# Kernel optimization log

Hardware: AMD Instinct MI355X
Metric: run time of the kernel (lower is better)

## Reference

```python
import jax, jax.numpy as jnp
import numpy as np

NUM_HEADS = 16
HEAD_DIM = 64  # hidden_size 1024 / 16 heads


def setup_inputs() -> dict:
    key = jax.random.key(0)
    ks = jax.random.split(key, 7)
    B, S, D = 32, 577, 1024
    s = 0.02
    return {
        "hidden_states": jax.random.normal(ks[0], (B, S, D), dtype=jnp.float32),
        "Wq": jax.random.normal(ks[1], (D, D), dtype=jnp.float32) * s,
        "bq": jax.random.normal(ks[2], (D,), dtype=jnp.float32) * s,
        "Wk": jax.random.normal(ks[3], (D, D), dtype=jnp.float32) * s,
        "bk": jax.random.normal(ks[4], (D,), dtype=jnp.float32) * s,
        "Wv": jax.random.normal(ks[5], (D, D), dtype=jnp.float32) * s,
        "bv": jax.random.normal(ks[6], (D,), dtype=jnp.float32) * s,
    }


def _split_heads(x):
    # [B, S, D] -> [B, H, S, d]
    B, S, D = x.shape
    return x.reshape(B, S, NUM_HEADS, HEAD_DIM).transpose(0, 2, 1, 3)


def reference(hidden_states, Wq, bq, Wk, bk, Wv, bv):
    # torch Linear: y = x @ W^T + b
    q = _split_heads(hidden_states @ Wq.T + bq)  # [B,H,S,d]
    k = _split_heads(hidden_states @ Wk.T + bk)
    v = _split_heads(hidden_states @ Wv.T + bv)

    scale = 1.0 / np.sqrt(HEAD_DIM).astype(np.float32)
    scores = jnp.einsum("bhqd,bhkd->bhqk", q, k) * scale  # [B,H,S,S]
    probs = jax.nn.softmax(scores, axis=-1)
    ctx = jnp.einsum("bhqk,bhkd->bhqd", probs, v)  # [B,H,S,d]
    B, H, S, d = ctx.shape
    ctx = ctx.transpose(0, 2, 1, 3).reshape(B, S, H * d)  # [B,S,D]
    return ctx
```

## Files before the change

kernel.cpp:

```cpp
#include <hip/hip_runtime.h>
#include <stdint.h>

#define NB 32
#define SEQ 577
#define SPAD 640
#define NH 16
#define HD 64
#define DM 1024
#define MTOT (NB * SEQ)
#define KT_N 16

typedef __bf16 bf16x8 __attribute__((ext_vector_type(8)));
typedef float f32x4 __attribute__((ext_vector_type(4)));
typedef unsigned short u16x8 __attribute__((ext_vector_type(8)));
typedef unsigned short u16x4 __attribute__((ext_vector_type(4)));

__device__ __forceinline__ unsigned short f2bf(float f) {
  unsigned int u = __builtin_bit_cast(unsigned int, f);
  return (unsigned short)((u + 0x7FFFu + ((u >> 16) & 1u)) >> 16);
}

__device__ __forceinline__ f32x4 mfma16(bf16x8 a, bf16x8 b, f32x4 c) {
  return __builtin_amdgcn_mfma_f32_16x16x32_bf16(a, b, c, 0, 0, 0);
}

__device__ __forceinline__ void gload16(const unsigned short* g, unsigned short* l) {
  __builtin_amdgcn_global_load_lds(
      (const __attribute__((address_space(1))) unsigned int*)g,
      (__attribute__((address_space(3))) unsigned int*)l, 16, 0, 0);
}

#define BC8(p) __builtin_bit_cast(bf16x8, *(const u16x8*)(p))

#if __has_builtin(__builtin_amdgcn_exp2f)
#define EXP2(x) __builtin_amdgcn_exp2f(x)
#else
#define EXP2(x) exp2f(x)
#endif

#define QSCALE 0.18033688f

__global__ void cvt_kernel(const float* __restrict__ x,
                           const float* __restrict__ wq,
                           const float* __restrict__ wk,
                           const float* __restrict__ wv,
                           unsigned short* __restrict__ xb,
                           unsigned short* __restrict__ wb) {
  const long long NX = (long long)MTOT * DM;
  long long i = ((long long)blockIdx.x * blockDim.x + threadIdx.x) * 4;
  const float* src;
  unsigned short* dst;
  if (i < NX) {
    src = x + i;
    dst = xb + i;
  } else {
    long long j = i - NX;
    int wsel = (int)(j >> 20);
    long long off = j & 0xFFFFF;
    src = (wsel == 0 ? wq : wsel == 1 ? wk : wv) + off;
    dst = wb + j;
  }
  f32x4 v = *(const f32x4*)src;
  u16x4 o;
  o.x = f2bf(v.x); o.y = f2bf(v.y); o.z = f2bf(v.z); o.w = f2bf(v.w);
  *(u16x4*)dst = o;
}

template <int MODE>
__device__ __forceinline__ void kloop256(
    unsigned short* LDS, const unsigned short* const* gA,
    const unsigned short* const* gB, f32x4 (&acc)[8][4],
    int rA0, int rB0, int ch0, int ch1) {
#define MM(ACC, AF, BF)                                   \
  do {                                                    \
    if constexpr (MODE == 0)                              \
      ACC = mfma16(AF, BF, ACC);                          \
    else                                                  \
      ACC = mfma16(BF, AF, ACC);                          \
  } while (0)
  const int t = threadIdx.x;
  for (int kt = 0; kt < KT_N; ++kt) {
    unsigned short* ab = LDS + (kt & 1) * 32768;
    unsigned short* bb = ab + 16384;
    const bool st = (kt + 2) < KT_N;
    const int ko2 = (kt + 2) * 64;
    bf16x8 af[4][2], bf0[2][2], bf1[2][2];

#pragma unroll
    for (int mi = 0; mi < 4; mi++) {
      const unsigned short* rp = ab + (rA0 + mi * 16) * 64;
      af[mi][0] = BC8(rp + ch0);
      af[mi][1] = BC8(rp + ch1);
    }
#pragma unroll
    for (int ni = 0; ni < 2; ni++) {
      const unsigned short* rp = bb + (rB0 + ni * 16) * 64;
      bf0[ni][0] = BC8(rp + ch0);
      bf0[ni][1] = BC8(rp + ch1);
    }
    __builtin_amdgcn_s_setprio(1);
#pragma unroll
    for (int mi = 0; mi < 4; mi++)
#pragma unroll
      for (int ni = 0; ni < 2; ni++) {
        MM(acc[mi][ni], af[mi][0], bf0[ni][0]);
        MM(acc[mi][ni], af[mi][1], bf0[ni][1]);
      }
    __builtin_amdgcn_s_setprio(0);
    asm volatile("s_waitcnt lgkmcnt(0)" ::: "memory");
    __builtin_amdgcn_s_barrier();
    __builtin_amdgcn_sched_barrier(0);

    if (st) {
      gload16(gA[0] + ko2, ab + 0 * 4096 + t * 8);
      gload16(gA[2] + ko2, ab + 2 * 4096 + t * 8);
    }
#pragma unroll
    for (int ni = 0; ni < 2; ni++) {
      const unsigned short* rp = bb + (rB0 + (2 + ni) * 16) * 64;
      bf1[ni][0] = BC8(rp + ch0);
      bf1[ni][1] = BC8(rp + ch1);
    }
    __builtin_amdgcn_s_setprio(1);
#pragma unroll
    for (int mi = 0; mi < 4; mi++)
#pragma unroll
      for (int ni = 0; ni < 2; ni++) {
        MM(acc[mi][2 + ni], af[mi][0], bf1[ni][0]);
        MM(acc[mi][2 + ni], af[mi][1], bf1[ni][1]);
      }
    __builtin_amdgcn_s_setprio(0);
    asm volatile("s_waitcnt lgkmcnt(0)" ::: "memory");
    __builtin_amdgcn_s_barrier();
    __builtin_amdgcn_sched_barrier(0);

    if (st) {
#pragma unroll
      for (int q = 0; q < 4; q++) gload16(gB[q] + ko2, bb + q * 4096 + t * 8);
    }
#pragma unroll
    for (int mi = 0; mi < 4; mi++) {
      const unsigned short* rp = ab + (rA0 + 64 + mi * 16) * 64;
      af[mi][0] = BC8(rp + ch0);
      af[mi][1] = BC8(rp + ch1);
    }
    __builtin_amdgcn_s_setprio(1);
#pragma unroll
    for (int mi = 0; mi < 4; mi++)
#pragma unroll
      for (int ni = 0; ni < 2; ni++) {
        MM(acc[4 + mi][2 + ni], af[mi][0], bf1[ni][0]);
        MM(acc[4 + mi][2 + ni], af[mi][1], bf1[ni][1]);
      }
    __builtin_amdgcn_s_setprio(0);
    asm volatile("s_waitcnt lgkmcnt(0)" ::: "memory");
    __builtin_amdgcn_s_barrier();
    __builtin_amdgcn_sched_barrier(0);

    if (st) {
      gload16(gA[1] + ko2, ab + 1 * 4096 + t * 8);
      gload16(gA[3] + ko2, ab + 3 * 4096 + t * 8);
    }
    __builtin_amdgcn_s_setprio(1);
#pragma unroll
    for (int mi = 0; mi < 4; mi++)
#pragma unroll
      for (int ni = 0; ni < 2; ni++) {
        MM(acc[4 + mi][ni], af[mi][0], bf0[ni][0]);
        MM(acc[4 + mi][ni], af[mi][1], bf0[ni][1]);
      }
    __builtin_amdgcn_s_setprio(0);
    if (kt == KT_N - 2)
      asm volatile("s_waitcnt vmcnt(0)" ::: "memory");
    else
      asm volatile("s_waitcnt vmcnt(8)" ::: "memory");
    __builtin_amdgcn_s_barrier();
    __builtin_amdgcn_sched_barrier(0);
  }
#undef MM
}

__global__ __launch_bounds__(512, 2) void gemm256u(
    const unsigned short* __restrict__ xb, const unsigned short* __restrict__ wb,
    const float* __restrict__ bq, const float* __restrict__ bk,
    const float* __restrict__ bv,
    unsigned short* __restrict__ qo, unsigned short* __restrict__ ko,
    unsigned short* __restrict__ vo) {
  __shared__ __align__(16) unsigned short LDS[65536];
  const int id = blockIdx.x;
  int m_tile, col, z;
  bool modeV;
  if (id < 584) {
    modeV = false;
    const int xcd = id & 7, j = id >> 3;
    const int p = xcd * 73 + j;
    m_tile = p >> 3;
    col = p & 7;
    z = col >> 2;
  } else {
    modeV = true;
    const int q = id - 584;
    const int xcd = q & 7, j = q >> 3;
    const int p = (xcd < 4) ? xcd * 37 + j : 148 + (xcd - 4) * 36 + j;
    m_tile = p >> 2;
    col = p & 3;
    z = 2;
  }
  const int n0 = (modeV ? col : (col & 3)) * 256;
  const int m0 = m_tile * 256;

  const int t = threadIdx.x;
  const int lane = t & 63;
  const int w = t >> 6;
  const int g = lane >> 4, c = lane & 15;
  const int wm = w & 1, wn = w >> 1;

  const unsigned short* W = wb + (size_t)z * (DM * DM);
  const float* bias = modeV ? bv : (z ? bk : bq);
  unsigned short* outp = modeV ? vo : (z ? ko : qo);
  const float qscale = (!modeV && z == 0) ? QSCALE : 1.0f;

  const int srow = t >> 3;
  const int schunk = (t & 7) ^ (srow & 7);
  const unsigned short* gA[4];
#pragma unroll
  for (int q = 0; q < 4; q++) {
    int rg = m0 + q * 64 + srow;
    if (rg > MTOT - 1) rg = MTOT - 1;
    gA[q] = xb + (size_t)rg * DM + schunk * 8;
  }
  const unsigned short* gB[4];
#pragma unroll
  for (int q = 0; q < 4; q++)
    gB[q] = W + (size_t)(n0 + q * 64 + srow) * DM + schunk * 8;

  const int cx = c & 7;
  const int ch0 = (g ^ cx) * 8;
  const int ch1 = ((4 + g) ^ cx) * 8;

  f32x4 acc[8][4];
#pragma unroll
  for (int mi = 0; mi < 8; mi++)
#pragma unroll
    for (int ni = 0; ni < 4; ni++) acc[mi][ni] = (f32x4)0.0f;

#pragma unroll
  for (int q = 0; q < 4; q++) gload16(gA[q], LDS + q * 4096 + t * 8);
#pragma unroll
  for (int q = 0; q < 4; q++) gload16(gB[q], LDS + 16384 + q * 4096 + t * 8);
#pragma unroll
  for (int q = 0; q < 4; q++) gload16(gA[q] + 64, LDS + 32768 + q * 4096 + t * 8);
#pragma unroll
  for (int q = 0; q < 4; q++)
    gload16(gB[q] + 64, LDS + 32768 + 16384 + q * 4096 + t * 8);
  asm volatile("s_waitcnt vmcnt(8)" ::: "memory");
  __builtin_amdgcn_s_barrier();
  __builtin_amdgcn_sched_barrier(0);

  const int rA0 = wm * 128 + c;
  const int rB0 = wn * 64 + c;

  if (!modeV)
    kloop256<0>(LDS, gA, gB, acc, rA0, rB0, ch0, ch1);
  else
    kloop256<1>(LDS, gA, gB, acc, rA0, rB0, ch0, ch1);

  if (!modeV) {
    float bias4[4];
#pragma unroll
    for (int ni = 0; ni < 4; ni++) bias4[ni] = bias[n0 + wn * 64 + ni * 16 + c];
#pragma unroll
    for (int mi = 0; mi < 8; mi++) {
      int mb = m0 + wm * 128 + mi * 16 + g * 4;
#pragma unroll
      for (int r = 0; r < 4; r++) {
        int m = mb + r;
        if (m >= MTOT) continue;
        int bi = m / SEQ;
        int s = m - bi * SEQ;
#pragma unroll
        for (int ni = 0; ni < 4; ni++) {
          int n = n0 + wn * 64 + ni * 16 + c;
          int hh = n >> 6, dd = n & 63;
          outp[(((size_t)bi * NH + hh) * SPAD + s) * HD + dd] =
              f2bf((acc[mi][ni][r] + bias4[ni]) * qscale);
        }
      }
    }
  } else {
#pragma unroll
    for (int ni = 0; ni < 4; ni++) {
#pragma unroll
      for (int r = 0; r < 4; r++) {
        int n = n0 + wn * 64 + ni * 16 + g * 4 + r;
        int hh = n >> 6, dd = n & 63;
        float bn = bias[n];
#pragma unroll
        for (int mi = 0; mi < 8; mi++) {
          int m = m0 + wm * 128 + mi * 16 + c;
          if (m >= MTOT) continue;
          int bi = m / SEQ;
          int s = m - bi * SEQ;
          outp[(((size_t)bi * NH + hh) * HD + dd) * SPAD + s] =
              f2bf(acc[mi][ni][r] + bn);
        }
      }
    }
  }
}

__global__ __launch_bounds__(256, 3) void attn_kernel(
    const unsigned short* __restrict__ Qb, const unsigned short* __restrict__ Kb,
    const unsigned short* __restrict__ Vt, float* __restrict__ out) {
  __shared__ __align__(16) unsigned short Ks[2][64 * 64];
  __shared__ __align__(16) unsigned short Vs[2][64 * 64];
  __shared__ __align__(16) unsigned short Vones[16 * 64];
  __shared__ __align__(16) unsigned short Pl[4][16 * 72];
  const int t = threadIdx.x, lane = t & 63, w = t >> 6;
  const int g = lane >> 4, c = lane & 15;

  const int id = blockIdx.x;
  const int xcd = id & 7;
  const int slot = id >> 3;
  const int qt = slot % 10;
  const int pairIdx = slot / 10;
  const int pair = xcd * 64 + pairIdx;
  const int b = pair >> 4;
  const int h = pair & 15;

  const int q0 = qt * 64 + w * 16;
  const size_t bh = (size_t)b * NH + h;
  const unsigned short* Qp = Qb + bh * SPAD * HD;
  const unsigned short* Kp = Kb + bh * SPAD * HD;
  const unsigned short* Vp = Vt + bh * HD * SPAD;

  {
    int rr = t >> 4, col = (t & 15) * 4;
    unsigned short val = (rr == 0) ? (unsigned short)0x3F80 : (unsigned short)0;
    u16x4 v4 = {val, val, val, val};
    *(u16x4*)(Vones + rr * 64 + col) = v4;
  }

  bf16x8 qf0 = __builtin_bit_cast(
      bf16x8, *(const u16x8*)(Qp + (size_t)(q0 + c) * HD + g * 8));
  bf16x8 qf1 = __builtin_bit_cast(
      bf16x8, *(const u16x8*)(Qp + (size_t)(q0 + c) * HD + 32 + g * 8));

  const int C0 = t, C1 = t + 256;
  const int r0 = C0 >> 3, cg0 = (C0 & 7) ^ (r0 & 7);
  const int r1 = C1 >> 3, cg1 = (C1 & 7) ^ (r1 & 7);
  const unsigned short* gK0 = Kp + (size_t)(r0 * 8 + cg0) * 8;
  const unsigned short* gK1 = Kp + (size_t)(r1 * 8 + cg1) * 8;
  const unsigned short* gV0 = Vp + (size_t)r0 * SPAD + cg0 * 8;
  const unsigned short* gV1 = Vp + (size_t)r1 * SPAD + cg1 * 8;

  f32x4 oacc[5];
#pragma unroll
  for (int nt = 0; nt < 5; nt++) oacc[nt] = (f32x4)0.0f;
  unsigned short* pl = &Pl[w][0];

  gload16(gK0, Ks[0] + C0 * 8);
  gload16(gK1, Ks[0] + C1 * 8);
  gload16(gV0, Vs[0] + C0 * 8);
  gload16(gV1, Vs[0] + C1 * 8);
  __syncthreads();

  for (int kt = 0; kt < 10; kt++) {
    const int cur = kt & 1, nxt = cur ^ 1;
    if (kt < 9) {
      const int kv1 = (kt + 1) * 64;
      gload16(gK0 + kv1 * 64, Ks[nxt] + C0 * 8);
      gload16(gK1 + kv1 * 64, Ks[nxt] + C1 * 8);
      gload16(gV0 + kv1, Vs[nxt] + C0 * 8);
      gload16(gV1 + kv1, Vs[nxt] + C1 * 8);
    }

    f32x4 sc[4];
    __builtin_amdgcn_s_setprio(1);
#pragma unroll
    for (int nt = 0; nt < 4; nt++) {
      const int row = nt * 16 + c;
      const unsigned short* kb = Ks[cur] + row * 64;
      bf16x8 k0 = __builtin_bit_cast(
          bf16x8, *(const u16x8*)(kb + ((g ^ (row & 7)) * 8)));
      bf16x8 k1 = __builtin_bit_cast(
          bf16x8, *(const u16x8*)(kb + (((4 + g) ^ (row & 7)) * 8)));
      sc[nt] = mfma16(qf0, k0, (f32x4)0.0f);
      sc[nt] = mfma16(qf1, k1, sc[nt]);
    }
    __builtin_amdgcn_s_setprio(0);

    if (kt == 9) {
      const int kv0 = kt * 64;
#pragma unroll
      for (int nt = 0; nt < 4; nt++) {
        const bool valid = (kv0 + nt * 16 + c) < SEQ;
#pragma unroll
        for (int r = 0; r < 4; r++)
          sc[nt][r] = valid ? EXP2(sc[nt][r]) : 0.0f;
      }
    } else {
#pragma unroll
      for (int nt = 0; nt < 4; nt++)
#pragma unroll
        for (int r = 0; r < 4; r++) sc[nt][r] = EXP2(sc[nt][r]);
    }

#pragma unroll
    for (int nt = 0; nt < 4; nt++)
#pragma unroll
      for (int r = 0; r < 4; r++)
        pl[(g * 4 + r) * 72 + nt * 16 + c] = f2bf(sc[nt][r]);
    bf16x8 pa0 = __builtin_bit_cast(bf16x8, *(const u16x8*)(pl + c * 72 + g * 8));
    bf16x8 pa1 =
        __builtin_bit_cast(bf16x8, *(const u16x8*)(pl + c * 72 + 32 + g * 8));

    __builtin_amdgcn_s_setprio(1);
#pragma unroll
    for (int nt = 0; nt < 5; nt++) {
      const int row = nt * 16 + c;
      const unsigned short* vb =
          (nt == 4) ? (Vones + c * 64) : (Vs[cur] + row * 64);
      bf16x8 v0 = __builtin_bit_cast(
          bf16x8, *(const u16x8*)(vb + ((g ^ (row & 7)) * 8)));
      bf16x8 v1 = __builtin_bit_cast(
          bf16x8, *(const u16x8*)(vb + (((4 + g) ^ (row & 7)) * 8)));
      oacc[nt] = mfma16(pa0, v0, oacc[nt]);
      oacc[nt] = mfma16(pa1, v1, oacc[nt]);
    }
    __builtin_amdgcn_s_setprio(0);

    __syncthreads();
  }

#pragma unroll
  for (int r = 0; r < 4; r++) {
    int s = q0 + g * 4 + r;
    if (s >= SEQ) continue;
    float l = __shfl(oacc[4][r], lane & 48, 64);
    float inv = 1.0f / l;
#pragma unroll
    for (int nt = 0; nt < 4; nt++)
      out[((size_t)b * SEQ + s) * DM + h * HD + nt * 16 + c] =
          oacc[nt][r] * inv;
  }
}

extern "C" void kernel_launch(void* const* d_in, const int* in_sizes, int n_in,
                              void* d_out, int out_size, void* d_ws,
                              size_t ws_size, hipStream_t stream) {
  const float* x = (const float*)d_in[0];
  const float* Wq = (const float*)d_in[1];
  const float* bq = (const float*)d_in[2];
  const float* Wk = (const float*)d_in[3];
  const float* bk = (const float*)d_in[4];
  const float* Wv = (const float*)d_in[5];
  const float* bv = (const float*)d_in[6];
  float* out = (float*)d_out;

  const size_t nXB = (size_t)MTOT * DM;
  const size_t nWB = (size_t)3 * DM * DM;
  const size_t nQK = (size_t)NB * NH * SPAD * HD;
  const size_t needed = (nXB + nWB + 3 * nQK) * 2;
  if (ws_size < needed) return;

  unsigned short* xb = (unsigned short*)d_ws;
  unsigned short* wb = xb + nXB;
  unsigned short* Qb = wb + nWB;
  unsigned short* Kb = Qb + nQK;
  unsigned short* Vt = Kb + nQK;

  cvt_kernel<<<21536, 256, 0, stream>>>(x, Wq, Wk, Wv, xb, wb);
  gemm256u<<<876, 512, 0, stream>>>(xb, wb, bq, bk, bv, Qb, Kb, Vt);
  attn_kernel<<<5120, 256, 0, stream>>>(Qb, Kb, Vt, out);
}
```

Measured before the change: 399.2 us.

## Replace 4-phase BK=64 GEMM pipeline with simple BK=32 double-buffered loop

The QKV projection GEMM main loop drops its interleaved four-phase schedule (BK=64, prefetch two tiles ahead, partial barriers between MFMA groups). In its place is a plain double-buffered loop with BK=32 that prefetches one tile ahead, then does all fragment loads and 32 MFMAs followed by a full vmcnt(0) wait and barrier. LDS use is halved and the swizzle changes to match 32-wide rows. The setprio hints in the attention kernel are also removed. The trade is simpler code and less LDS against twice as many barriers and a shallower latency-hiding pipeline.

```diff
diff --git a/kernel.cpp b/kernel.cpp
--- a/kernel.cpp
+++ b/kernel.cpp
@@ -8,7 +8,7 @@
 #define HD 64
 #define DM 1024
 #define MTOT (NB * SEQ)
-#define KT_N 16
+#define NKT 32
 
 typedef __bf16 bf16x8 __attribute__((ext_vector_type(8)));
 typedef float f32x4 __attribute__((ext_vector_type(4)));
@@ -67,10 +67,10 @@
 }
 
 template <int MODE>
-__device__ __forceinline__ void kloop256(
+__device__ __forceinline__ void kloop32(
     unsigned short* LDS, const unsigned short* const* gA,
     const unsigned short* const* gB, f32x4 (&acc)[8][4],
-    int rA0, int rB0, int ch0, int ch1) {
+    int rA0, int rB0, int chA) {
 #define MM(ACC, AF, BF)                                   \
   do {                                                    \
     if constexpr (MODE == 0)                              \
@@ -79,101 +79,30 @@
       ACC = mfma16(BF, AF, ACC);                          \
   } while (0)
   const int t = threadIdx.x;
-  for (int kt = 0; kt < KT_N; ++kt) {
-    unsigned short* ab = LDS + (kt & 1) * 32768;
-    unsigned short* bb = ab + 16384;
-    const bool st = (kt + 2) < KT_N;
-    const int ko2 = (kt + 2) * 64;
-    bf16x8 af[4][2], bf0[2][2], bf1[2][2];
-
-#pragma unroll
-    for (int mi = 0; mi < 4; mi++) {
-      const unsigned short* rp = ab + (rA0 + mi * 16) * 64;
-      af[mi][0] = BC8(rp + ch0);
-      af[mi][1] = BC8(rp + ch1);
-    }
-#pragma unroll
-    for (int ni = 0; ni < 2; ni++) {
-      const unsigned short* rp = bb + (rB0 + ni * 16) * 64;
-      bf0[ni][0] = BC8(rp + ch0);
-      bf0[ni][1] = BC8(rp + ch1);
-    }
+  for (int kt = 0; kt < NKT; ++kt) {
+    unsigned short* bufc = LDS + (kt & 1) * 16384;
+    unsigned short* bufn = LDS + ((kt & 1) ^ 1) * 16384;
+    if (kt + 1 < NKT) {
+      const int k1 = (kt + 1) * 32;
+      gload16(gA[0] + k1, bufn + t * 8);
+      gload16(gA[1] + k1, bufn + 4096 + t * 8);
+      gload16(gB[0] + k1, bufn + 8192 + t * 8);
+      gload16(gB[1] + k1, bufn + 12288 + t * 8);
+    }
+    bf16x8 af[8], bfr[4];
+#pragma unroll
+    for (int mi = 0; mi < 8; mi++)
+      af[mi] = BC8(bufc + (rA0 + mi * 16) * 32 + chA);
+#pragma unroll
+    for (int ni = 0; ni < 4; ni++)
+      bfr[ni] = BC8(bufc + 8192 + (rB0 + ni * 16) * 32 + chA);
     __builtin_amdgcn_s_setprio(1);
 #pragma unroll
-    for (int mi = 0; mi < 4; mi++)
-#pragma unroll
-      for (int ni = 0; ni < 2; ni++) {
-        MM(acc[mi][ni], af[mi][0], bf0[ni][0]);
-        MM(acc[mi][ni], af[mi][1], bf0[ni][1]);
-      }
+    for (int mi = 0; mi < 8; mi++)
+#pragma unroll
+      for (int ni = 0; ni < 4; ni++) MM(acc[mi][ni], af[mi], bfr[ni]);
     __builtin_amdgcn_s_setprio(0);
-    asm volatile("s_waitcnt lgkmcnt(0)" ::: "memory");
-    __builtin_amdgcn_s_barrier();
-    __builtin_amdgcn_sched_barrier(0);
-
-    if (st) {
-      gload16(gA[0] + ko2, ab + 0 * 4096 + t * 8);
-      gload16(gA[2] + ko2, ab + 2 * 4096 + t * 8);
-    }
-#pragma unroll
-    for (int ni = 0; ni < 2; ni++) {
-      const unsigned short* rp = bb + (rB0 + (2 + ni) * 16) * 64;
-      bf1[ni][0] = BC8(rp + ch0);
-      bf1[ni][1] = BC8(rp + ch1);
-    }
-    __builtin_amdgcn_s_setprio(1);
-#pragma unroll
-    for (int mi = 0; mi < 4; mi++)
-#pragma unroll
-      for (int ni = 0; ni < 2; ni++) {
-        MM(acc[mi][2 + ni], af[mi][0], bf1[ni][0]);
-        MM(acc[mi][2 + ni], af[mi][1], bf1[ni][1]);
-      }
-    __builtin_amdgcn_s_setprio(0);
-    asm volatile("s_waitcnt lgkmcnt(0)" ::: "memory");
-    __builtin_amdgcn_s_barrier();
-    __builtin_amdgcn_sched_barrier(0);
-
-    if (st) {
-#pragma unroll
-      for (int q = 0; q < 4; q++) gload16(gB[q] + ko2, bb + q * 4096 + t * 8);
-    }
-#pragma unroll
-    for (int mi = 0; mi < 4; mi++) {
-      const unsigned short* rp = ab + (rA0 + 64 + mi * 16) * 64;
-      af[mi][0] = BC8(rp + ch0);
-      af[mi][1] = BC8(rp + ch1);
-    }
-    __builtin_amdgcn_s_setprio(1);
-#pragma unroll
-    for (int mi = 0; mi < 4; mi++)
-#pragma unroll
-      for (int ni = 0; ni < 2; ni++) {
-        MM(acc[4 + mi][2 + ni], af[mi][0], bf1[ni][0]);
-        MM(acc[4 + mi][2 + ni], af[mi][1], bf1[ni][1]);
-      }
-    __builtin_amdgcn_s_setprio(0);
-    asm volatile("s_waitcnt lgkmcnt(0)" ::: "memory");
-    __builtin_amdgcn_s_barrier();
-    __builtin_amdgcn_sched_barrier(0);
-
-    if (st) {
-      gload16(gA[1] + ko2, ab + 1 * 4096 + t * 8);
-      gload16(gA[3] + ko2, ab + 3 * 4096 + t * 8);
-    }
-    __builtin_amdgcn_s_setprio(1);
-#pragma unroll
-    for (int mi = 0; mi < 4; mi++)
-#pragma unroll
-      for (int ni = 0; ni < 2; ni++) {
-        MM(acc[4 + mi][ni], af[mi][0], bf0[ni][0]);
-        MM(acc[4 + mi][ni], af[mi][1], bf0[ni][1]);
-      }
-    __builtin_amdgcn_s_setprio(0);
-    if (kt == KT_N - 2)
-      asm volatile("s_waitcnt vmcnt(0)" ::: "memory");
-    else
-      asm volatile("s_waitcnt vmcnt(8)" ::: "memory");
+    asm volatile("s_waitcnt vmcnt(0)" ::: "memory");
     __builtin_amdgcn_s_barrier();
     __builtin_amdgcn_sched_barrier(0);
   }
@@ -186,7 +115,7 @@
     const float* __restrict__ bv,
     unsigned short* __restrict__ qo, unsigned short* __restrict__ ko,
     unsigned short* __restrict__ vo) {
-  __shared__ __align__(16) unsigned short LDS[65536];
+  __shared__ __align__(16) unsigned short LDS[32768];
   const int id = blockIdx.x;
   int m_tile, col, z;
   bool modeV;
@@ -220,23 +149,22 @@
   unsigned short* outp = modeV ? vo : (z ? ko : qo);
   const float qscale = (!modeV && z == 0) ? QSCALE : 1.0f;
 
-  const int srow = t >> 3;
-  const int schunk = (t & 7) ^ (srow & 7);
-  const unsigned short* gA[4];
-#pragma unroll
-  for (int q = 0; q < 4; q++) {
-    int rg = m0 + q * 64 + srow;
-    if (rg > MTOT - 1) rg = MTOT - 1;
-    gA[q] = xb + (size_t)rg * DM + schunk * 8;
-  }
-  const unsigned short* gB[4];
-#pragma unroll
-  for (int q = 0; q < 4; q++)
-    gB[q] = W + (size_t)(n0 + q * 64 + srow) * DM + schunk * 8;
-
-  const int cx = c & 7;
-  const int ch0 = (g ^ cx) * 8;
-  const int ch1 = ((4 + g) ^ cx) * 8;
+  const int srow = t >> 2;
+  const int sswz = (t & 3) ^ (srow & 3);
+  const unsigned short* gA[2];
+  {
+    int r0_ = m0 + srow;       if (r0_ > MTOT - 1) r0_ = MTOT - 1;
+    int r1_ = m0 + 128 + srow; if (r1_ > MTOT - 1) r1_ = MTOT - 1;
+    gA[0] = xb + (size_t)r0_ * DM + sswz * 8;
+    gA[1] = xb + (size_t)r1_ * DM + sswz * 8;
+  }
+  const unsigned short* gB[2];
+  gB[0] = W + (size_t)(n0 + srow) * DM + sswz * 8;
+  gB[1] = W + (size_t)(n0 + 128 + srow) * DM + sswz * 8;
+
+  const int chA = (g ^ (c & 3)) * 8;
+  const int rA0 = wm * 128 + c;
+  const int rB0 = wn * 64 + c;
 
   f32x4 acc[8][4];
 #pragma unroll
@@ -244,26 +172,18 @@
 #pragma unroll
     for (int ni = 0; ni < 4; ni++) acc[mi][ni] = (f32x4)0.0f;
 
-#pragma unroll
-  for (int q = 0; q < 4; q++) gload16(gA[q], LDS + q * 4096 + t * 8);
-#pragma unroll
-  for (int q = 0; q < 4; q++) gload16(gB[q], LDS + 16384 + q * 4096 + t * 8);
-#pragma unroll
-  for (int q = 0; q < 4; q++) gload16(gA[q] + 64, LDS + 32768 + q * 4096 + t * 8);
-#pragma unroll
-  for (int q = 0; q < 4; q++)
-    gload16(gB[q] + 64, LDS + 32768 + 16384 + q * 4096 + t * 8);
-  asm volatile("s_waitcnt vmcnt(8)" ::: "memory");
+  gload16(gA[0], LDS + t * 8);
+  gload16(gA[1], LDS + 4096 + t * 8);
+  gload16(gB[0], LDS + 8192 + t * 8);
+  gload16(gB[1], LDS + 12288 + t * 8);
+  asm volatile("s_waitcnt vmcnt(0)" ::: "memory");
   __builtin_amdgcn_s_barrier();
   __builtin_amdgcn_sched_barrier(0);
 
-  const int rA0 = wm * 128 + c;
-  const int rB0 = wn * 64 + c;
-
   if (!modeV)
-    kloop256<0>(LDS, gA, gB, acc, rA0, rB0, ch0, ch1);
+    kloop32<0>(LDS, gA, gB, acc, rA0, rB0, chA);
   else
-    kloop256<1>(LDS, gA, gB, acc, rA0, rB0, ch0, ch1);
+    kloop32<1>(LDS, gA, gB, acc, rA0, rB0, chA);
 
   if (!modeV) {
     float bias4[4];
@@ -376,7 +296,6 @@
     }
 
     f32x4 sc[4];
-    __builtin_amdgcn_s_setprio(1);
 #pragma unroll
     for (int nt = 0; nt < 4; nt++) {
       const int row = nt * 16 + c;
@@ -388,7 +307,6 @@
       sc[nt] = mfma16(qf0, k0, (f32x4)0.0f);
       sc[nt] = mfma16(qf1, k1, sc[nt]);
     }
-    __builtin_amdgcn_s_setprio(0);
 
     if (kt == 9) {
       const int kv0 = kt * 64;
@@ -415,7 +333,6 @@
     bf16x8 pa1 =
         __builtin_bit_cast(bf16x8, *(const u16x8*)(pl + c * 72 + 32 + g * 8));
 
-    __builtin_amdgcn_s_setprio(1);
 #pragma unroll
     for (int nt = 0; nt < 5; nt++) {
       const int row = nt * 16 + c;
@@ -428,7 +345,6 @@
       oacc[nt] = mfma16(pa0, v0, oacc[nt]);
       oacc[nt] = mfma16(pa1, v1, oacc[nt]);
     }
-    __builtin_amdgcn_s_setprio(0);
 
     __syncthreads();
   }
```

After: 415.8 us. 4.2% more time.

## Transpose score MFMA so softmax row sums accumulate in registers

Applied to the files above, without the earlier changes.

The QK^T MFMA operands are swapped so each lane holds the scores of a single query. The softmax denominator is then summed in registers and reduced with two cross-lane shuffles, which replaces the extra ones-matrix MFMA column and its LDS buffer. P is written to LDS as packed 4-element bf16 chunks with an XOR swizzle instead of scalar stores into a padded layout. The setprio hints are dropped and launch bounds are raised to 4 blocks per SM, which trades register headroom for occupancy.

```diff
diff --git a/kernel.cpp b/kernel.cpp
--- a/kernel.cpp
+++ b/kernel.cpp
@@ -309,13 +309,12 @@
   }
 }
 
-__global__ __launch_bounds__(256, 3) void attn_kernel(
+__global__ __launch_bounds__(256, 4) void attn_kernel(
     const unsigned short* __restrict__ Qb, const unsigned short* __restrict__ Kb,
     const unsigned short* __restrict__ Vt, float* __restrict__ out) {
   __shared__ __align__(16) unsigned short Ks[2][64 * 64];
   __shared__ __align__(16) unsigned short Vs[2][64 * 64];
-  __shared__ __align__(16) unsigned short Vones[16 * 64];
-  __shared__ __align__(16) unsigned short Pl[4][16 * 72];
+  __shared__ __align__(16) unsigned short Pl[4][16 * 64];
   const int t = threadIdx.x, lane = t & 63, w = t >> 6;
   const int g = lane >> 4, c = lane & 15;
 
@@ -334,13 +333,6 @@
   const unsigned short* Kp = Kb + bh * SPAD * HD;
   const unsigned short* Vp = Vt + bh * HD * SPAD;
 
-  {
-    int rr = t >> 4, col = (t & 15) * 4;
-    unsigned short val = (rr == 0) ? (unsigned short)0x3F80 : (unsigned short)0;
-    u16x4 v4 = {val, val, val, val};
-    *(u16x4*)(Vones + rr * 64 + col) = v4;
-  }
-
   bf16x8 qf0 = __builtin_bit_cast(
       bf16x8, *(const u16x8*)(Qp + (size_t)(q0 + c) * HD + g * 8));
   bf16x8 qf1 = __builtin_bit_cast(
@@ -354,10 +346,16 @@
   const unsigned short* gV0 = Vp + (size_t)r0 * SPAD + cg0 * 8;
   const unsigned short* gV1 = Vp + (size_t)r1 * SPAD + cg1 * 8;
 
-  f32x4 oacc[5];
-#pragma unroll
-  for (int nt = 0; nt < 5; nt++) oacc[nt] = (f32x4)0.0f;
+  f32x4 oacc[4];
+#pragma unroll
+  for (int nt = 0; nt < 4; nt++) oacc[nt] = (f32x4)0.0f;
+  float lsum = 0.0f;
   unsigned short* pl = &Pl[w][0];
+
+  const int pbase = c * 64;
+  const int psw2 = (c & 7) << 1;
+  const int rd0 = (g ^ (c & 7)) * 8;
+  const int rd1 = ((4 + g) ^ (c & 7)) * 8;
 
   gload16(gK0, Ks[0] + C0 * 8);
   gload16(gK1, Ks[0] + C1 * 8);
@@ -376,7 +374,6 @@
     }
 
     f32x4 sc[4];
-    __builtin_amdgcn_s_setprio(1);
 #pragma unroll
     for (int nt = 0; nt < 4; nt++) {
       const int row = nt * 16 + c;
@@ -385,20 +382,18 @@
           bf16x8, *(const u16x8*)(kb + ((g ^ (row & 7)) * 8)));
       bf16x8 k1 = __builtin_bit_cast(
           bf16x8, *(const u16x8*)(kb + (((4 + g) ^ (row & 7)) * 8)));
-      sc[nt] = mfma16(qf0, k0, (f32x4)0.0f);
-      sc[nt] = mfma16(qf1, k1, sc[nt]);
-    }
-    __builtin_amdgcn_s_setprio(0);
+      sc[nt] = mfma16(k0, qf0, (f32x4)0.0f);
+      sc[nt] = mfma16(k1, qf1, sc[nt]);
+    }
 
     if (kt == 9) {
-      const int kv0 = kt * 64;
-#pragma unroll
-      for (int nt = 0; nt < 4; nt++) {
-        const bool valid = (kv0 + nt * 16 + c) < SEQ;
-#pragma unroll
-        for (int r = 0; r < 4; r++)
+#pragma unroll
+      for (int nt = 0; nt < 4; nt++)
+#pragma unroll
+        for (int r = 0; r < 4; r++) {
+          const bool valid = (576 + nt * 16 + g * 4 + r) < SEQ;
           sc[nt][r] = valid ? EXP2(sc[nt][r]) : 0.0f;
-      }
+        }
     } else {
 #pragma unroll
       for (int nt = 0; nt < 4; nt++)
@@ -407,20 +402,21 @@
     }
 
 #pragma unroll
-    for (int nt = 0; nt < 4; nt++)
-#pragma unroll
-      for (int r = 0; r < 4; r++)
-        pl[(g * 4 + r) * 72 + nt * 16 + c] = f2bf(sc[nt][r]);
-    bf16x8 pa0 = __builtin_bit_cast(bf16x8, *(const u16x8*)(pl + c * 72 + g * 8));
-    bf16x8 pa1 =
-        __builtin_bit_cast(bf16x8, *(const u16x8*)(pl + c * 72 + 32 + g * 8));
-
-    __builtin_amdgcn_s_setprio(1);
-#pragma unroll
-    for (int nt = 0; nt < 5; nt++) {
+    for (int nt = 0; nt < 4; nt++) {
+      lsum += sc[nt][0] + sc[nt][1] + sc[nt][2] + sc[nt][3];
+      unsigned pk0 = (unsigned)f2bf(sc[nt][0]) | ((unsigned)f2bf(sc[nt][1]) << 16);
+      unsigned pk1 = (unsigned)f2bf(sc[nt][2]) | ((unsigned)f2bf(sc[nt][3]) << 16);
+      const int ch4 = (nt * 4 + g) ^ psw2;
+      uint2 pv2 = {pk0, pk1};
+      *(uint2*)(pl + pbase + ch4 * 4) = pv2;
+    }
+    bf16x8 pa0 = BC8(pl + pbase + rd0);
+    bf16x8 pa1 = BC8(pl + pbase + rd1);
+
+#pragma unroll
+    for (int nt = 0; nt < 4; nt++) {
       const int row = nt * 16 + c;
-      const unsigned short* vb =
-          (nt == 4) ? (Vones + c * 64) : (Vs[cur] + row * 64);
+      const unsigned short* vb = Vs[cur] + row * 64;
       bf16x8 v0 = __builtin_bit_cast(
           bf16x8, *(const u16x8*)(vb + ((g ^ (row & 7)) * 8)));
       bf16x8 v1 = __builtin_bit_cast(
@@ -428,16 +424,18 @@
       oacc[nt] = mfma16(pa0, v0, oacc[nt]);
       oacc[nt] = mfma16(pa1, v1, oacc[nt]);
     }
-    __builtin_amdgcn_s_setprio(0);
 
     __syncthreads();
   }
+
+  lsum += __shfl_xor(lsum, 16, 64);
+  lsum += __shfl_xor(lsum, 32, 64);
 
 #pragma unroll
   for (int r = 0; r < 4; r++) {
     int s = q0 + g * 4 + r;
     if (s >= SEQ) continue;
-    float l = __shfl(oacc[4][r], lane & 48, 64);
+    float l = __shfl(lsum, (lane & 48) | (g * 4 + r), 64);
     float inv = 1.0f / l;
 #pragma unroll
     for (int nt = 0; nt < 4; nt++)
```

Result: faster. 391.0 us (-2.1%).
